# Kernel tuning notes

Measured on AMD Instinct MI355X. Metric: run time of the kernel, lower is better.

The kernel has to match this reference:

```python
import jax, jax.numpy as jnp
import numpy as np

TAU = 20.0
TH = 1.0
TAU_THETA = 50.0
THETA_INC = 0.5
REFRAC_STEPS = 5
K = 10.0  # surrogate sigmoid sharpness
B, L = 65536, 400


def setup_inputs() -> dict:
    key = jax.random.key(0)
    I = jax.random.normal(key, (B, L), dtype=jnp.float32)
    return {"I": I}


def _lif_forward(I):
    Bn, Ln = I.shape
    dt = I.dtype

    def step(carry, I_t):
        v, theta, ref = carry
        # Euler membrane update: v += -v/tau + I_t
        v = v + (-v / TAU + I_t)
        can_spike = (ref == 0)
        x = v - theta
        s_soft = jax.nn.sigmoid(K * x) * can_spike.astype(dt)
        s_hard = ((x >= 0.0) & can_spike).astype(dt)
        # straight-through: value = s_hard, gradient flows through s_soft
        s = jax.lax.stop_gradient(s_hard - s_soft) + s_soft
        ref = jnp.where(s_hard > 0, jnp.int32(REFRAC_STEPS), jnp.maximum(ref - 1, 0))
        # reset uses detached spike (multiplier is a constant wrt grad)
        v = v * (1.0 - jax.lax.stop_gradient(s))
        # adaptive threshold: decay to base + bump on hard spike
        theta = theta - (theta - TH) / TAU_THETA + THETA_INC * s_hard
        return (v, theta, ref), (s, s_hard)

    init = (jnp.zeros((Bn,), dt), jnp.full((Bn,), TH, dt), jnp.zeros((Bn,), jnp.int32))
    _, (spikes_t, hard_t) = jax.lax.scan(step, init, jnp.swapaxes(I, 0, 1))
    spikes = jnp.swapaxes(spikes_t, 0, 1)       # [B, L]
    hard_spikes = jnp.swapaxes(hard_t, 0, 1)    # [B, L]
    return spikes, hard_spikes


def _soft_lat(spikes):
    Ln = spikes.shape[1]
    time = jnp.arange(Ln, dtype=spikes.dtype)
    w = spikes / (spikes.sum(axis=1, keepdims=True) + 1e-6)
    return (w * time).sum(axis=1)


def reference(I):
    spikes, hard_spikes = _lif_forward(I)
    fired = hard_spikes > 0.5
    has_spike = jnp.any(fired, axis=1)
    first_idx = jnp.argmax(fired, axis=1)
    hard_latency = jnp.where(has_spike, first_idx, I.shape[1]).astype(jnp.int64)
    soft_latency = _soft_lat(spikes)
    return spikes, hard_latency, soft_latency
```

## Files before the change

### kernel.cpp

```cpp
#include <hip/hip_runtime.h>


constexpr int Bsz  = 65536;
constexpr int Lsz  = 400;
constexpr int ROWS = 64;
constexpr int TC   = 40;
constexpr int STRIDE = 41;
constexpr int V4   = TC / 4;

typedef float floatx4 __attribute__((ext_vector_type(4)));

__device__ __forceinline__ int sumpos(unsigned int w) {
    return __popc(w & 0xAAAAAAAAu) + (__popc(w & 0xCCCCCCCCu) << 1) +
           (__popc(w & 0xF0F0F0F0u) << 2) + (__popc(w & 0xFF00FF00u) << 3) +
           (__popc(w & 0xFFFF0000u) << 4);
}

__global__ __launch_bounds__(2 * ROWS)
void lif_kernel(const float* __restrict__ I, float* __restrict__ out)
{
    __shared__ float in2[2][ROWS * STRIDE];
    __shared__ unsigned int bits[2][ROWS * 4];

    const int tid  = threadIdx.x;
    const int wv   = tid >> 6;
    const int lane = tid & 63;
    const int rb   = blockIdx.x * ROWS;

    if (wv == 1) {
        const float* Ib = I   + (size_t)rb * Lsz;
        float*       Sb = out + (size_t)rb * Lsz;
        float4 rg[V4];

        auto issue = [&](int ch) {
#pragma unroll
            for (int k = 0; k < V4; ++k) {
                const int idx = k * 64 + lane;
                const int r   = idx / V4;
                const int c4  = idx % V4;
                rg[k] = *reinterpret_cast<const float4*>(
                            Ib + (size_t)r * Lsz + ch * TC + c4 * 4);
            }
        };
        auto put = [&](int buf) {
#pragma unroll
            for (int k = 0; k < V4; ++k) {
                const int idx = k * 64 + lane;
                const int r   = idx / V4;
                const int c4  = idx % V4;
                float* d = &in2[buf][r * STRIDE + c4 * 4];
                d[0] = rg[k].x; d[1] = rg[k].y; d[2] = rg[k].z; d[3] = rg[k].w;
            }
        };
        auto expand_half = [&](int pair, int half) {
            const unsigned int* bl = bits[pair & 1];
#pragma unroll
            for (int q = 0; q < 10; ++q) {
                const int it  = half * 10 + q;
                const int idx = it * ROWS + lane;
                const int r   = idx / 20;
                const int c4  = idx % 20;
                const unsigned int word = bl[r * 4 + (c4 >> 3)];
                const int bb = (c4 & 7) * 4;
                floatx4 vv = { (float)((word >> (bb + 0)) & 1u),
                               (float)((word >> (bb + 1)) & 1u),
                               (float)((word >> (bb + 2)) & 1u),
                               (float)((word >> (bb + 3)) & 1u) };
                __builtin_nontemporal_store(vv,
                    reinterpret_cast<floatx4*>(Sb + (size_t)r * Lsz + pair * 80 + c4 * 4));
            }
        };

        issue(0); put(0); issue(1);
        __syncthreads();
        for (int pr = 0; pr < 5; ++pr) {
            const int ch = 2 * pr;
            put(1);
            if (ch + 2 < 10) issue(ch + 2);
            if (pr >= 1) expand_half(pr - 1, 0);
            __syncthreads();
            if (ch + 2 < 10) put(0);
            if (ch + 3 < 10) issue(ch + 3);
            if (pr >= 1) expand_half(pr - 1, 1);
            __syncthreads();
        }
        expand_half(4, 0); expand_half(4, 1);
    } else {
        float v = 0.0f, theta = 1.0f;
        int allow = 0, first = Lsz;
        int cnt_i = 0, swt_i = 0;
        unsigned int w0, w1, w2;

        auto scan_chunk = [&](int buf, int t0, int gb) {
            const float* src = &in2[buf][lane * STRIDE];
            float rg[TC];
#pragma unroll
            for (int c = 0; c < TC; ++c) rg[c] = src[c];
#pragma unroll
            for (int c = 0; c < TC; ++c) {
                v = __builtin_fmaf(v, 0.95f, rg[c]);
                const int t = t0 + c;
                const bool hard = (v >= theta) & (t >= allow);
                v     = hard ? 0.0f : v;
                theta = __builtin_fmaf(theta, 0.98f, hard ? 0.52f : 0.02f);
                allow = hard ? (t + 6) : allow;
                const int cg = gb + c;
                const unsigned int m = hard ? (1u << (cg & 31)) : 0u;
                if (cg < 32) w0 |= m; else if (cg < 64) w1 |= m; else w2 |= m;
            }
        };

        __syncthreads();
        for (int pr = 0; pr < 5; ++pr) {
            w0 = w1 = w2 = 0u;
            scan_chunk(0, 2 * pr * TC, 0);
            __syncthreads();
            scan_chunk(1, (2 * pr + 1) * TC, TC);
            const int tp = pr * 80;
            const int p0 = __popc(w0), p1 = __popc(w1), p2 = __popc(w2);
            const int cp = p0 + p1 + p2;
            cnt_i += cp;
            swt_i += tp * cp + sumpos(w0) + sumpos(w1) + 32 * p1 +
                     sumpos(w2) + 64 * p2;
            const int cand = w0 ? tp + (__ffs(w0) - 1)
                           : w1 ? tp + 32 + (__ffs(w1) - 1)
                           : w2 ? tp + 64 + (__ffs(w2) - 1) : Lsz;
            first = min(first, cand);
            *reinterpret_cast<uint4*>(&bits[pr & 1][lane * 4]) =
                make_uint4(w0, w1, w2, 0u);
            __syncthreads();
        }
        const int row = rb + lane;
        out[(size_t)Bsz * Lsz + row]       = (float)first;
        out[(size_t)Bsz * Lsz + Bsz + row] = (float)swt_i / ((float)cnt_i + 1e-6f);
    }
}

extern "C" void kernel_launch(void* const* d_in, const int* in_sizes, int n_in,
                              void* d_out, int out_size, void* d_ws, size_t ws_size,
                              hipStream_t stream)
{
    const float* I = (const float*)d_in[0];
    float* out = (float*)d_out;
    lif_kernel<<<dim3(Bsz / ROWS), dim3(2 * ROWS), 0, stream>>>(I, out);
}
```

Before: 36.85 us.

## Use global_load_lds DMA with XOR-swizzled LDS layout for input staging

Replaces the register-staged global loads and scalar LDS stores in the producer wave with direct global-to-LDS DMA via global_load_lds, removing the padded stride. To avoid bank conflicts without padding, the global source columns are XOR-swizzled per row group and the consumer wave reads float4 vectors with the matching inverse swizzle. This cuts VGPR use and per-element LDS writes in the producer. It relies on the DMA's lane-contiguous LDS placement matching the swizzle, and on the barriers covering completion of the asynchronous loads.

```diff
diff --git a/kernel.cpp b/kernel.cpp
--- a/kernel.cpp
+++ b/kernel.cpp
@@ -5,7 +5,6 @@
 constexpr int Lsz  = 400;
 constexpr int ROWS = 64;
 constexpr int TC   = 40;
-constexpr int STRIDE = 41;
 constexpr int V4   = TC / 4;
 
 typedef float floatx4 __attribute__((ext_vector_type(4)));
@@ -16,10 +15,18 @@
            (__popc(w & 0xFFFF0000u) << 4);
 }
 
+__device__ __forceinline__ void dma16(const float* g, float* l)
+{
+    __builtin_amdgcn_global_load_lds(
+        (const __attribute__((address_space(1))) void*)g,
+        (__attribute__((address_space(3))) void*)l,
+        16, 0, 0);
+}
+
 __global__ __launch_bounds__(2 * ROWS)
 void lif_kernel(const float* __restrict__ I, float* __restrict__ out)
 {
-    __shared__ float in2[2][ROWS * STRIDE];
+    __shared__ float in2[2][ROWS * TC];
     __shared__ unsigned int bits[2][ROWS * 4];
 
     const int tid  = threadIdx.x;
@@ -30,27 +37,20 @@
     if (wv == 1) {
         const float* Ib = I   + (size_t)rb * Lsz;
         float*       Sb = out + (size_t)rb * Lsz;
-        float4 rg[V4];
 
-        auto issue = [&](int ch) {
+        int goff[V4];
 #pragma unroll
-            for (int k = 0; k < V4; ++k) {
-                const int idx = k * 64 + lane;
-                const int r   = idx / V4;
-                const int c4  = idx % V4;
-                rg[k] = *reinterpret_cast<const float4*>(
-                            Ib + (size_t)r * Lsz + ch * TC + c4 * 4);
-            }
-        };
-        auto put = [&](int buf) {
+        for (int k = 0; k < V4; ++k) {
+            const int s  = k * 64 + lane;
+            const int r  = s / 10;
+            const int jp = s % 10;
+            const int jg = (jp < 8) ? (jp ^ ((r >> 2) & 7)) : jp;
+            goff[k] = r * Lsz + jg * 4;
+        }
+        auto dma = [&](int ch, int buf) {
 #pragma unroll
-            for (int k = 0; k < V4; ++k) {
-                const int idx = k * 64 + lane;
-                const int r   = idx / V4;
-                const int c4  = idx % V4;
-                float* d = &in2[buf][r * STRIDE + c4 * 4];
-                d[0] = rg[k].x; d[1] = rg[k].y; d[2] = rg[k].z; d[3] = rg[k].w;
-            }
+            for (int k = 0; k < V4; ++k)
+                dma16(Ib + goff[k] + ch * TC, &in2[buf][k * 256]);
         };
         auto expand_half = [&](int pair, int half) {
             const unsigned int* bl = bits[pair & 1];
@@ -71,16 +71,14 @@
             }
         };
 
-        issue(0); put(0); issue(1);
+        dma(0, 0);
         __syncthreads();
         for (int pr = 0; pr < 5; ++pr) {
             const int ch = 2 * pr;
-            put(1);
-            if (ch + 2 < 10) issue(ch + 2);
+            dma(ch + 1, 1);
             if (pr >= 1) expand_half(pr - 1, 0);
             __syncthreads();
-            if (ch + 2 < 10) put(0);
-            if (ch + 3 < 10) issue(ch + 3);
+            if (ch + 2 < 10) dma(ch + 2, 0);
             if (pr >= 1) expand_half(pr - 1, 1);
             __syncthreads();
         }
@@ -90,15 +88,20 @@
         int allow = 0, first = Lsz;
         int cnt_i = 0, swt_i = 0;
         unsigned int w0, w1, w2;
+        const int gl = (lane >> 2) & 7;
 
         auto scan_chunk = [&](int buf, int t0, int gb) {
-            const float* src = &in2[buf][lane * STRIDE];
-            float rg[TC];
+            const float* src = &in2[buf][lane * TC];
+            float4 rgc4[V4];
 #pragma unroll
-            for (int c = 0; c < TC; ++c) rg[c] = src[c];
+            for (int j = 0; j < V4; ++j) {
+                const int jj = (j < 8) ? (j ^ gl) : j;
+                rgc4[j] = *reinterpret_cast<const float4*>(src + jj * 4);
+            }
+            const float* in = reinterpret_cast<const float*>(rgc4);
 #pragma unroll
             for (int c = 0; c < TC; ++c) {
-                v = __builtin_fmaf(v, 0.95f, rg[c]);
+                v = __builtin_fmaf(v, 0.95f, in[c]);
                 const int t = t0 + c;
                 const bool hard = (v >= theta) & (t >= allow);
                 v     = hard ? 0.0f : v;
```

New measurement: 35.56 us (median of 2 runs). -3.5%, faster.
